# Kernel optimization log

Hardware: AMD Instinct MI355X
Metric: run time of the kernel (lower is better)

## Reference

```python
import jax, jax.numpy as jnp
import numpy as np

_D, _H, _W = 8, 56, 56
WS = 3
PAD = WS // 2
NUM_HEADS = 8
DIM = 128
HEAD_DIM = DIM // NUM_HEADS
LOCAL_LEN = WS ** 3
OFFSETS = [(dz, dy, dx) for dz in range(WS) for dy in range(WS) for dx in range(WS)]


def _mask_and_scale():
    # Replicates get_seqlen_and_mask: which of the 27 neighbors are in-bounds.
    z = np.arange(_D)[:, None, None]
    y = np.arange(_H)[None, :, None]
    x = np.arange(_W)[None, None, :]
    valid = []
    for dz, dy, dx in OFFSETS:
        v = ((z + dz - PAD >= 0) & (z + dz - PAD < _D) &
             (y + dy - PAD >= 0) & (y + dy - PAD < _H) &
             (x + dx - PAD >= 0) & (x + dx - PAD < _W))
        valid.append(np.broadcast_to(v, (_D, _H, _W)).reshape(-1))
    valid = np.stack(valid, -1)  # [N, 27]
    pad_mask = jnp.asarray(~valid)  # True where neighbor is padding
    seq_scale = jnp.asarray(np.log(valid.sum(-1).astype(np.float32))[:, None])  # [N, 1]
    return pad_mask, seq_scale

PAD_MASK, SEQ_SCALE = _mask_and_scale()


def _l2norm(t):
    # F.normalize(dim=-1) with eps=1e-12
    return t / jnp.maximum(jnp.linalg.norm(t, axis=-1, keepdims=True), 1e-12)


def setup_inputs() -> dict:
    key = jax.random.key(0)
    ks = jax.random.split(key, 8)
    B, N, C = 4, _D * _H * _W, DIM
    s = 0.02
    return {
        "x": jax.random.normal(ks[0], (B, N, C), jnp.float32),
        "q_w": jax.random.normal(ks[1], (C, C), jnp.float32) * s,
        "q_b": jnp.zeros((C,), jnp.float32),
        "kv_w": jax.random.normal(ks[2], (2 * C, C), jnp.float32) * s,
        "kv_b": jnp.zeros((2 * C,), jnp.float32),
        "proj_w": jax.random.normal(ks[3], (C, C), jnp.float32) * s,
        "proj_b": jnp.zeros((C,), jnp.float32),
        "temperature": jnp.log(jnp.expm1(jnp.ones((NUM_HEADS, 1, 1), jnp.float32) / 0.24)),
        "query_embedding": jax.random.normal(ks[4], (NUM_HEADS, 1, HEAD_DIM), jnp.float32) * 0.02,
        "rel_pos_bias": jax.random.normal(ks[5], (NUM_HEADS, LOCAL_LEN), jnp.float32) * 0.0004,
        "D": _D, "H": _H, "W": _W,
    }


def reference(x, q_w, q_b, kv_w, kv_b, proj_w, proj_b, temperature,
              query_embedding, rel_pos_bias, D, H, W):
    B, N, C = x.shape
    h, hd = NUM_HEADS, HEAD_DIM

    # q branch: linear -> per-head L2 normalize -> embed/temperature/length scaling
    q = (x @ q_w.T + q_b).reshape(B, N, h, hd).transpose(0, 2, 1, 3)  # [B,h,N,hd]
    q = _l2norm(q)
    q = (q + query_embedding) * jax.nn.softplus(temperature) * SEQ_SCALE

    # kv branch: k L2-normalized per head, v raw
    kv = x @ kv_w.T + kv_b
    k, v = kv[..., :C], kv[..., C:]
    k = _l2norm(k.reshape(B, N, h, hd))
    kmap = k.transpose(0, 2, 3, 1).reshape(B, h, hd, D, H, W)
    vmap = v.reshape(B, N, h, hd).transpose(0, 2, 3, 1).reshape(B, h, hd, D, H, W)
    pad_cfg = [(0, 0)] * 3 + [(PAD, PAD)] * 3
    kpad = jnp.pad(kmap, pad_cfg)
    vpad = jnp.pad(vmap, pad_cfg)

    # QK over 27 shifted views == unfold3d gather without materializing [B,h,hd,27,N]
    attn = []
    for dz, dy, dx in OFFSETS:
        ks = kpad[..., dz:dz + D, dy:dy + H, dx:dx + W].reshape(B, h, hd, N)
        attn.append(jnp.einsum('bhnd,bhdn->bhn', q, ks))
    attn = jnp.stack(attn, -1)  # [B,h,N,27]
    attn = attn + rel_pos_bias[None, :, None, :]
    attn = jnp.where(PAD_MASK[None, None], -jnp.inf, attn)
    attn = jax.nn.softmax(attn, axis=-1)

    # AV accumulation over the same 27 shifts
    out = jnp.zeros((B, h, N, hd), x.dtype)
    for j, (dz, dy, dx) in enumerate(OFFSETS):
        vs = vpad[..., dz:dz + D, dy:dy + H, dx:dx + W].reshape(B, h, hd, N)
        out = out + attn[..., j, None] * vs.transpose(0, 1, 3, 2)
    out = out.transpose(0, 2, 1, 3).reshape(B, N, C)
    return out @ proj_w.T + proj_b
```

## Files before the change

### kernel.cpp

```cpp
#include <hip/hip_runtime.h>

#define DD 8
#define HH 56
#define WW 56
#define HWW (HH*WW)
#define NTOK (DD*HH*WW)
#define BB 4
#define CC 128
#define NH 8
#define HD 16
#define MTOT (BB*NTOK)

__device__ __forceinline__ unsigned short f2bf(float f){
    unsigned int u = __float_as_uint(f);
    u += 0x7FFFu + ((u>>16)&1u);
    return (unsigned short)(u>>16);
}
__device__ __forceinline__ float bf2f(unsigned short s){
    return __uint_as_float(((unsigned int)s)<<16);
}

__global__ __launch_bounds__(256)
void qkv_kernel(const float* __restrict__ x,
                const float* __restrict__ qw, const float* __restrict__ qb,
                const float* __restrict__ kvw, const float* __restrict__ kvb,
                const float* __restrict__ temp, const float* __restrict__ qemb,
                float* __restrict__ qbuf, float* __restrict__ kbuf,
                unsigned short* __restrict__ vbuf)
{
    __shared__ float xs[32*72];
    __shared__ float wsl[32*388];
    const int t = threadIdx.x;
    const int rowbase = blockIdx.x * 64;
    const int r0 = 4*(t>>4);
    const int c0 = 4*(t&15);

    float acc[4][24];
    #pragma unroll
    for (int cc=0; cc<6; ++cc){
        #pragma unroll
        for (int j=0;j<4;++j){
            int col = cc*64 + c0 + j;
            float b = (col<CC) ? qb[col] : kvb[col-CC];
            #pragma unroll
            for (int i=0;i<4;++i) acc[i][cc*4+j]=b;
        }
    }

    for (int ks=0; ks<4; ++ks){
        __syncthreads();
        #pragma unroll
        for (int i=0;i<2;++i){
            int id = 4*t + 1024*i;
            int row = id>>5, k0 = id&31;
            float4 xv = *reinterpret_cast<const float4*>(x + (size_t)(rowbase+row)*CC + ks*32 + k0);
            xs[(k0+0)*72+row]=xv.x; xs[(k0+1)*72+row]=xv.y;
            xs[(k0+2)*72+row]=xv.z; xs[(k0+3)*72+row]=xv.w;
        }
        #pragma unroll
        for (int i=0;i<12;++i){
            int id = 4*t + 1024*i;
            int c = id>>5, k0 = id&31;
            const float* wrow = (c<CC) ? (qw + (size_t)c*CC) : (kvw + (size_t)(c-CC)*CC);
            float4 wv = *reinterpret_cast<const float4*>(wrow + ks*32 + k0);
            wsl[(k0+0)*388+c]=wv.x; wsl[(k0+1)*388+c]=wv.y;
            wsl[(k0+2)*388+c]=wv.z; wsl[(k0+3)*388+c]=wv.w;
        }
        __syncthreads();
        #pragma unroll 4
        for (int k=0;k<32;++k){
            float4 xa = *reinterpret_cast<const float4*>(&xs[k*72 + r0]);
            float xr[4] = {xa.x, xa.y, xa.z, xa.w};
            #pragma unroll
            for (int cc=0;cc<6;++cc){
                float4 wb = *reinterpret_cast<const float4*>(&wsl[k*388 + cc*64 + c0]);
                float wr[4] = {wb.x,wb.y,wb.z,wb.w};
                #pragma unroll
                for (int i=0;i<4;++i){
                    #pragma unroll
                    for (int j=0;j<4;++j)
                        acc[i][cc*4+j] = fmaf(xr[i], wr[j], acc[i][cc*4+j]);
                }
            }
        }
    }

    #pragma unroll
    for (int cc=0; cc<6; ++cc){
        const int sel = cc>>1;
        const int colbase = (cc&1)*64 + c0;
        float vals[4][4];
        #pragma unroll
        for (int i=0;i<4;++i){
            #pragma unroll
            for (int j=0;j<4;++j) vals[i][j]=acc[i][cc*4+j];
        }

        if (sel<2){
            #pragma unroll
            for (int i=0;i<4;++i){
                float s = vals[i][0]*vals[i][0]+vals[i][1]*vals[i][1]
                        + vals[i][2]*vals[i][2]+vals[i][3]*vals[i][3];
                s += __shfl_xor(s,1);
                s += __shfl_xor(s,2);
                float inv = 1.0f/fmaxf(sqrtf(s),1e-12f);
                #pragma unroll
                for (int j=0;j<4;++j) vals[i][j]*=inv;
            }
        }
        if (sel==0){
            const int head = colbase>>4;
            const int d0 = colbase&15;
            float tm = temp[head];
            float sps = (tm>15.f)?tm:log1pf(__expf(tm));
            float qe[4];
            #pragma unroll
            for (int j=0;j<4;++j) qe[j]=qemb[head*HD + d0 + j];
            #pragma unroll
            for (int i=0;i<4;++i){
                int row = rowbase + r0 + i;
                int n = row % NTOK;
                int z = n / HWW; int rem = n - z*HWW;
                int y = rem / WW; int xx = rem - y*WW;
                int cnt = (3-(z==0)-(z==DD-1))*(3-(y==0)-(y==HH-1))*(3-(xx==0)-(xx==WW-1));
                float sc = logf((float)cnt) * sps;
                #pragma unroll
                for (int j=0;j<4;++j) vals[i][j]=(vals[i][j]+qe[j])*sc;
            }
        }
        #pragma unroll
        for (int i=0;i<4;++i){
            int row = rowbase + r0 + i;
            if (sel==0){
                *reinterpret_cast<float4*>(qbuf + (size_t)row*CC + colbase)
                    = make_float4(vals[i][0],vals[i][1],vals[i][2],vals[i][3]);
            } else if (sel==1){
                *reinterpret_cast<float4*>(kbuf + (size_t)row*CC + colbase)
                    = make_float4(vals[i][0],vals[i][1],vals[i][2],vals[i][3]);
            } else {
                *reinterpret_cast<ushort4*>(vbuf + (size_t)row*CC + colbase)
                    = make_ushort4(f2bf(vals[i][0]),f2bf(vals[i][1]),f2bf(vals[i][2]),f2bf(vals[i][3]));
            }
        }
    }
}

__global__ __launch_bounds__(256)
void attn_kernel(float* __restrict__ qa,
                 const float* __restrict__ kbuf,
                 const unsigned short* __restrict__ vbuf,
                 const float* __restrict__ rpb)
{
    const int t = threadIdx.x;
    const int tok = blockIdx.x*32 + (t>>3);
    const int h = t&7;
    const int n = tok % NTOK;
    const int z = n / HWW; const int rem = n - z*HWW;
    const int y = rem / WW; const int xx = rem - y*WW;
    const int tokbase = tok - n;

    float qf[16];
    {
        const float4* qp = reinterpret_cast<const float4*>(qa + (size_t)tok*CC + h*HD);
        float4 a=qp[0],b=qp[1],c=qp[2],d=qp[3];
        qf[0]=a.x;qf[1]=a.y;qf[2]=a.z;qf[3]=a.w;
        qf[4]=b.x;qf[5]=b.y;qf[6]=b.z;qf[7]=b.w;
        qf[8]=c.x;qf[9]=c.y;qf[10]=c.z;qf[11]=c.w;
        qf[12]=d.x;qf[13]=d.y;qf[14]=d.z;qf[15]=d.w;
    }

    float l[27];
    #pragma unroll
    for (int j=0;j<27;++j){
        const int dz=j/9, dy=(j/3)%3, dx=j%3;
        int z2=z+dz-1, y2=y+dy-1, x2=xx+dx-1;
        bool valid = ((unsigned)z2<DD) && ((unsigned)y2<HH) && ((unsigned)x2<WW);
        int row2 = valid ? (tokbase + z2*HWW + y2*WW + x2) : tok;
        const float4* kp = reinterpret_cast<const float4*>(kbuf + (size_t)row2*CC + h*HD);
        float4 ka=kp[0],kb=kp[1],kc=kp[2],kd=kp[3];
        float kk[16]={ka.x,ka.y,ka.z,ka.w, kb.x,kb.y,kb.z,kb.w,
                      kc.x,kc.y,kc.z,kc.w, kd.x,kd.y,kd.z,kd.w};
        float s = 0.f;
        #pragma unroll
        for (int d=0;d<16;++d) s = fmaf(qf[d],kk[d],s);
        l[j] = valid ? (s + rpb[h*27+j]) : -1e30f;
    }

    float m = l[0];
    #pragma unroll
    for (int j=1;j<27;++j) m = fmaxf(m,l[j]);
    float sum=0.f;
    #pragma unroll
    for (int j=0;j<27;++j){ float e=__expf(l[j]-m); l[j]=e; sum+=e; }
    float rs = 1.0f/sum;

    float o[16];
    #pragma unroll
    for (int d=0;d<16;++d) o[d]=0.f;
    #pragma unroll
    for (int j=0;j<27;++j){
        const int dz=j/9, dy=(j/3)%3, dx=j%3;
        int z2=z+dz-1, y2=y+dy-1, x2=xx+dx-1;
        bool valid = ((unsigned)z2<DD) && ((unsigned)y2<HH) && ((unsigned)x2<WW);
        int row2 = valid ? (tokbase + z2*HWW + y2*WW + x2) : tok;
        const uint4* vp = reinterpret_cast<const uint4*>(vbuf + (size_t)row2*CC + h*HD);
        uint4 va=vp[0], vb=vp[1];
        unsigned int vw[8]={va.x,va.y,va.z,va.w,vb.x,vb.y,vb.z,vb.w};
        float w = l[j];
        #pragma unroll
        for (int q2=0;q2<8;++q2){
            o[2*q2]   = fmaf(w, bf2f((unsigned short)(vw[q2]&0xffffu)), o[2*q2]);
            o[2*q2+1] = fmaf(w, bf2f((unsigned short)(vw[q2]>>16)),     o[2*q2+1]);
        }
    }
    #pragma unroll
    for (int d=0;d<16;++d) o[d]*=rs;
    float4* op = reinterpret_cast<float4*>(qa + (size_t)tok*CC + h*HD);
    op[0]=make_float4(o[0],o[1],o[2],o[3]);
    op[1]=make_float4(o[4],o[5],o[6],o[7]);
    op[2]=make_float4(o[8],o[9],o[10],o[11]);
    op[3]=make_float4(o[12],o[13],o[14],o[15]);
}

__global__ __launch_bounds__(256)
void proj_kernel(const float* __restrict__ ao, const float* __restrict__ pw,
                 const float* __restrict__ pb, float* __restrict__ out)
{
    __shared__ float xs[32*72];
    __shared__ float wsl[32*132];
    const int t = threadIdx.x;
    const int rowbase = blockIdx.x*64;
    const int r0 = 4*(t>>4);
    const int c0 = 8*(t&15);
    float acc[4][8];
    #pragma unroll
    for (int j=0;j<8;++j){
        float b=pb[c0+j];
        #pragma unroll
        for (int i=0;i<4;++i) acc[i][j]=b;
    }
    for (int ks=0;ks<4;++ks){
        __syncthreads();
        #pragma unroll
        for (int i=0;i<2;++i){
            int id=4*t+1024*i; int row=id>>5,k0=id&31;
            float4 xv = *reinterpret_cast<const float4*>(ao + (size_t)(rowbase+row)*CC + ks*32 + k0);
            xs[(k0+0)*72+row]=xv.x; xs[(k0+1)*72+row]=xv.y;
            xs[(k0+2)*72+row]=xv.z; xs[(k0+3)*72+row]=xv.w;
        }
        #pragma unroll
        for (int i=0;i<4;++i){
            int id=4*t+1024*i; int c=id>>5,k0=id&31;
            float4 wv = *reinterpret_cast<const float4*>(pw + (size_t)c*CC + ks*32 + k0);
            wsl[(k0+0)*132+c]=wv.x; wsl[(k0+1)*132+c]=wv.y;
            wsl[(k0+2)*132+c]=wv.z; wsl[(k0+3)*132+c]=wv.w;
        }
        __syncthreads();
        #pragma unroll 4
        for (int k=0;k<32;++k){
            float4 xa=*reinterpret_cast<const float4*>(&xs[k*72+r0]);
            float xr[4]={xa.x,xa.y,xa.z,xa.w};
            float4 w0=*reinterpret_cast<const float4*>(&wsl[k*132+c0]);
            float4 w1=*reinterpret_cast<const float4*>(&wsl[k*132+c0+4]);
            float wr[8]={w0.x,w0.y,w0.z,w0.w,w1.x,w1.y,w1.z,w1.w};
            #pragma unroll
            for (int i=0;i<4;++i){
                #pragma unroll
                for (int j=0;j<8;++j)
                    acc[i][j] = fmaf(xr[i], wr[j], acc[i][j]);
            }
        }
    }
    #pragma unroll
    for (int i=0;i<4;++i){
        int row=rowbase+r0+i;
        *reinterpret_cast<float4*>(out+(size_t)row*CC+c0)
            = make_float4(acc[i][0],acc[i][1],acc[i][2],acc[i][3]);
        *reinterpret_cast<float4*>(out+(size_t)row*CC+c0+4)
            = make_float4(acc[i][4],acc[i][5],acc[i][6],acc[i][7]);
    }
}

extern "C" void kernel_launch(void* const* d_in, const int* in_sizes, int n_in,
                              void* d_out, int out_size, void* d_ws, size_t ws_size,
                              hipStream_t stream)
{
    const float* x    = (const float*)d_in[0];
    const float* qw   = (const float*)d_in[1];
    const float* qb   = (const float*)d_in[2];
    const float* kvw  = (const float*)d_in[3];
    const float* kvb  = (const float*)d_in[4];
    const float* pw   = (const float*)d_in[5];
    const float* pb   = (const float*)d_in[6];
    const float* temp = (const float*)d_in[7];
    const float* qemb = (const float*)d_in[8];
    const float* rpb  = (const float*)d_in[9];

    float* qbuf = (float*)d_ws;
    float* kbuf = qbuf + (size_t)MTOT*CC;
    unsigned short* vbuf = (unsigned short*)(kbuf + (size_t)MTOT*CC);

    hipLaunchKernelGGL(qkv_kernel, dim3(MTOT/64), dim3(256), 0, stream,
                       x,qw,qb,kvw,kvb,temp,qemb,qbuf,kbuf,vbuf);
    hipLaunchKernelGGL(attn_kernel, dim3(MTOT/32), dim3(256), 0, stream,
                       qbuf,kbuf,vbuf,rpb);
    hipLaunchKernelGGL(proj_kernel, dim3(MTOT/64), dim3(256), 0, stream,
                       qbuf,pw,pb,(float*)d_out);
}
```

Before: 485.9 us.

## Use split-bf16 MFMA for QKV and output projection GEMMs

Replaces the scalar FP32 FMA GEMMs in the qkv and projection kernels with bf16 MFMA 16x16x32 instructions. Precision is kept close to FP32 by splitting operands into hi/lo bf16 parts, using three MFMAs per tile. A small pre-kernel splits the weights each call, and activations are split in registers without shared memory staging. This trades FP32 ALU work for matrix-core throughput, at the cost of an extra launch, strided scalar stores in the epilogue, and an approximation slightly less exact than FP32.

```diff
diff --git a/kernel.cpp b/kernel.cpp
--- a/kernel.cpp
+++ b/kernel.cpp
@@ -11,6 +11,9 @@
 #define HD 16
 #define MTOT (BB*NTOK)
 
+typedef __attribute__((ext_vector_type(8))) short bf16x8;
+typedef __attribute__((ext_vector_type(4))) float f32x4;
+
 __device__ __forceinline__ unsigned short f2bf(float f){
     unsigned int u = __float_as_uint(f);
     u += 0x7FFFu + ((u>>16)&1u);
@@ -21,125 +24,144 @@
 }
 
 __global__ __launch_bounds__(256)
+void wsplit_kernel(const float* __restrict__ qw, const float* __restrict__ kvw,
+                   const float* __restrict__ pw,
+                   unsigned short* __restrict__ whi, unsigned short* __restrict__ wlo,
+                   unsigned short* __restrict__ pwhi, unsigned short* __restrict__ pwlo)
+{
+    int idx = blockIdx.x*256 + threadIdx.x;
+    if (idx < 49152){
+        float s = (idx < 16384) ? qw[idx] : kvw[idx-16384];
+        unsigned short h = f2bf(s);
+        unsigned short l = f2bf(s - bf2f(h));
+        whi[idx]=h; wlo[idx]=l;
+    } else {
+        int j = idx - 49152;
+        float s = pw[j];
+        unsigned short h = f2bf(s);
+        unsigned short l = f2bf(s - bf2f(h));
+        pwhi[j]=h; pwlo[j]=l;
+    }
+}
+
+__global__ __launch_bounds__(256)
 void qkv_kernel(const float* __restrict__ x,
-                const float* __restrict__ qw, const float* __restrict__ qb,
-                const float* __restrict__ kvw, const float* __restrict__ kvb,
+                const float* __restrict__ qb, const float* __restrict__ kvb,
+                const unsigned short* __restrict__ whi, const unsigned short* __restrict__ wlo,
                 const float* __restrict__ temp, const float* __restrict__ qemb,
                 float* __restrict__ qbuf, float* __restrict__ kbuf,
                 unsigned short* __restrict__ vbuf)
 {
-    __shared__ float xs[32*72];
-    __shared__ float wsl[32*388];
-    const int t = threadIdx.x;
-    const int rowbase = blockIdx.x * 64;
-    const int r0 = 4*(t>>4);
-    const int c0 = 4*(t&15);
-
-    float acc[4][24];
-    #pragma unroll
-    for (int cc=0; cc<6; ++cc){
-        #pragma unroll
-        for (int j=0;j<4;++j){
-            int col = cc*64 + c0 + j;
-            float b = (col<CC) ? qb[col] : kvb[col-CC];
-            #pragma unroll
-            for (int i=0;i<4;++i) acc[i][cc*4+j]=b;
-        }
-    }
-
+    const int t  = threadIdx.x;
+    const int wv = t>>6;
+    const int l  = t&63;
+    const int lr = l&15;
+    const int lg = l>>4;
+    const int m0 = blockIdx.x*64;
+
+    f32x4 acc[4][6];
+    #pragma unroll
+    for (int j=0;j<6;++j){
+        int col = (wv*6+j)*16 + lr;
+        float b = (col<CC) ? qb[col] : kvb[col-CC];
+        #pragma unroll
+        for (int rt=0;rt<4;++rt) acc[rt][j] = (f32x4){b,b,b,b};
+    }
+
+    #pragma unroll
     for (int ks=0; ks<4; ++ks){
-        __syncthreads();
-        #pragma unroll
-        for (int i=0;i<2;++i){
-            int id = 4*t + 1024*i;
-            int row = id>>5, k0 = id&31;
-            float4 xv = *reinterpret_cast<const float4*>(x + (size_t)(rowbase+row)*CC + ks*32 + k0);
-            xs[(k0+0)*72+row]=xv.x; xs[(k0+1)*72+row]=xv.y;
-            xs[(k0+2)*72+row]=xv.z; xs[(k0+3)*72+row]=xv.w;
-        }
-        #pragma unroll
-        for (int i=0;i<12;++i){
-            int id = 4*t + 1024*i;
-            int c = id>>5, k0 = id&31;
-            const float* wrow = (c<CC) ? (qw + (size_t)c*CC) : (kvw + (size_t)(c-CC)*CC);
-            float4 wv = *reinterpret_cast<const float4*>(wrow + ks*32 + k0);
-            wsl[(k0+0)*388+c]=wv.x; wsl[(k0+1)*388+c]=wv.y;
-            wsl[(k0+2)*388+c]=wv.z; wsl[(k0+3)*388+c]=wv.w;
-        }
-        __syncthreads();
-        #pragma unroll 4
-        for (int k=0;k<32;++k){
-            float4 xa = *reinterpret_cast<const float4*>(&xs[k*72 + r0]);
-            float xr[4] = {xa.x, xa.y, xa.z, xa.w};
-            #pragma unroll
-            for (int cc=0;cc<6;++cc){
-                float4 wb = *reinterpret_cast<const float4*>(&wsl[k*388 + cc*64 + c0]);
-                float wr[4] = {wb.x,wb.y,wb.z,wb.w};
+        bf16x8 ahi[4], alo[4];
+        #pragma unroll
+        for (int rt=0;rt<4;++rt){
+            const float* xp = x + (size_t)(m0 + rt*16 + lr)*CC + ks*32 + lg*8;
+            float4 xa = *reinterpret_cast<const float4*>(xp);
+            float4 xb = *reinterpret_cast<const float4*>(xp+4);
+            float xf[8] = {xa.x,xa.y,xa.z,xa.w, xb.x,xb.y,xb.z,xb.w};
+            #pragma unroll
+            for (int jj=0;jj<8;++jj){
+                unsigned short h = f2bf(xf[jj]);
+                unsigned short lo2 = f2bf(xf[jj] - bf2f(h));
+                ahi[rt][jj] = (short)h;
+                alo[rt][jj] = (short)lo2;
+            }
+        }
+        #pragma unroll
+        for (int j=0;j<6;++j){
+            const int c = (wv*6+j)*16 + lr;
+            const size_t off = (size_t)c*CC + ks*32 + lg*8;
+            bf16x8 bhi = *reinterpret_cast<const bf16x8*>(whi + off);
+            bf16x8 blo = *reinterpret_cast<const bf16x8*>(wlo + off);
+            #pragma unroll
+            for (int rt=0;rt<4;++rt){
+                acc[rt][j] = __builtin_amdgcn_mfma_f32_16x16x32_bf16(ahi[rt], bhi, acc[rt][j], 0,0,0);
+                acc[rt][j] = __builtin_amdgcn_mfma_f32_16x16x32_bf16(alo[rt], bhi, acc[rt][j], 0,0,0);
+                acc[rt][j] = __builtin_amdgcn_mfma_f32_16x16x32_bf16(ahi[rt], blo, acc[rt][j], 0,0,0);
+            }
+        }
+    }
+
+    float slog[4][4];
+    #pragma unroll
+    for (int rt=0;rt<4;++rt){
+        #pragma unroll
+        for (int r=0;r<4;++r){
+            int row = m0 + rt*16 + lg*4 + r;
+            int n = row % NTOK;
+            int z = n / HWW; int rem = n - z*HWW;
+            int y = rem / WW; int xx = rem - y*WW;
+            const float L2 = 0.69314718f, L3 = 1.09861229f;
+            float sl = ((z==0||z==DD-1)?L2:L3) + ((y==0||y==HH-1)?L2:L3) + ((xx==0||xx==WW-1)?L2:L3);
+            slog[rt][r] = sl;
+        }
+    }
+
+    #pragma unroll
+    for (int j=0;j<6;++j){
+        const int ct  = wv*6+j;
+        const int sel = ct>>3;
+        const int head = ct & 7;
+        float vals[4][4];
+        #pragma unroll
+        for (int rt=0;rt<4;++rt){
+            #pragma unroll
+            for (int r=0;r<4;++r) vals[rt][r] = acc[rt][j][r];
+        }
+        if (sel < 2){
+            #pragma unroll
+            for (int rt=0;rt<4;++rt){
                 #pragma unroll
-                for (int i=0;i<4;++i){
-                    #pragma unroll
-                    for (int j=0;j<4;++j)
-                        acc[i][cc*4+j] = fmaf(xr[i], wr[j], acc[i][cc*4+j]);
+                for (int r=0;r<4;++r){
+                    float s = vals[rt][r]*vals[rt][r];
+                    s += __shfl_xor(s,1); s += __shfl_xor(s,2);
+                    s += __shfl_xor(s,4); s += __shfl_xor(s,8);
+                    float inv = 1.0f/fmaxf(sqrtf(s),1e-12f);
+                    vals[rt][r] *= inv;
                 }
             }
         }
-    }
-
-    #pragma unroll
-    for (int cc=0; cc<6; ++cc){
-        const int sel = cc>>1;
-        const int colbase = (cc&1)*64 + c0;
-        float vals[4][4];
-        #pragma unroll
-        for (int i=0;i<4;++i){
-            #pragma unroll
-            for (int j=0;j<4;++j) vals[i][j]=acc[i][cc*4+j];
-        }
-
-        if (sel<2){
-            #pragma unroll
-            for (int i=0;i<4;++i){
-                float s = vals[i][0]*vals[i][0]+vals[i][1]*vals[i][1]
-                        + vals[i][2]*vals[i][2]+vals[i][3]*vals[i][3];
-                s += __shfl_xor(s,1);
-                s += __shfl_xor(s,2);
-                float inv = 1.0f/fmaxf(sqrtf(s),1e-12f);
-                #pragma unroll
-                for (int j=0;j<4;++j) vals[i][j]*=inv;
-            }
-        }
-        if (sel==0){
-            const int head = colbase>>4;
-            const int d0 = colbase&15;
+        if (sel == 0){
             float tm = temp[head];
             float sps = (tm>15.f)?tm:log1pf(__expf(tm));
-            float qe[4];
-            #pragma unroll
-            for (int j=0;j<4;++j) qe[j]=qemb[head*HD + d0 + j];
-            #pragma unroll
-            for (int i=0;i<4;++i){
-                int row = rowbase + r0 + i;
-                int n = row % NTOK;
-                int z = n / HWW; int rem = n - z*HWW;
-                int y = rem / WW; int xx = rem - y*WW;
-                int cnt = (3-(z==0)-(z==DD-1))*(3-(y==0)-(y==HH-1))*(3-(xx==0)-(xx==WW-1));
-                float sc = logf((float)cnt) * sps;
+            float qe = qemb[head*HD + lr];
+            #pragma unroll
+            for (int rt=0;rt<4;++rt){
                 #pragma unroll
-                for (int j=0;j<4;++j) vals[i][j]=(vals[i][j]+qe[j])*sc;
-            }
-        }
-        #pragma unroll
-        for (int i=0;i<4;++i){
-            int row = rowbase + r0 + i;
-            if (sel==0){
-                *reinterpret_cast<float4*>(qbuf + (size_t)row*CC + colbase)
-                    = make_float4(vals[i][0],vals[i][1],vals[i][2],vals[i][3]);
-            } else if (sel==1){
-                *reinterpret_cast<float4*>(kbuf + (size_t)row*CC + colbase)
-                    = make_float4(vals[i][0],vals[i][1],vals[i][2],vals[i][3]);
-            } else {
-                *reinterpret_cast<ushort4*>(vbuf + (size_t)row*CC + colbase)
-                    = make_ushort4(f2bf(vals[i][0]),f2bf(vals[i][1]),f2bf(vals[i][2]),f2bf(vals[i][3]));
+                for (int r=0;r<4;++r)
+                    vals[rt][r] = (vals[rt][r]+qe)*(slog[rt][r]*sps);
+            }
+        }
+        #pragma unroll
+        for (int rt=0;rt<4;++rt){
+            #pragma unroll
+            for (int r=0;r<4;++r){
+                int row = m0 + rt*16 + lg*4 + r;
+                if (sel==0){
+                    qbuf[(size_t)row*CC + ct*16 + lr] = vals[rt][r];
+                } else if (sel==1){
+                    kbuf[(size_t)row*CC + (ct-8)*16 + lr] = vals[rt][r];
+                } else {
+                    vbuf[(size_t)row*CC + (ct-16)*16 + lr] = f2bf(vals[rt][r]);
+                }
             }
         }
     }
@@ -223,61 +245,68 @@
 }
 
 __global__ __launch_bounds__(256)
-void proj_kernel(const float* __restrict__ ao, const float* __restrict__ pw,
+void proj_kernel(const float* __restrict__ ao,
+                 const unsigned short* __restrict__ pwhi, const unsigned short* __restrict__ pwlo,
                  const float* __restrict__ pb, float* __restrict__ out)
 {
-    __shared__ float xs[32*72];
-    __shared__ float wsl[32*132];
-    const int t = threadIdx.x;
-    const int rowbase = blockIdx.x*64;
-    const int r0 = 4*(t>>4);
-    const int c0 = 8*(t&15);
-    float acc[4][8];
-    #pragma unroll
-    for (int j=0;j<8;++j){
-        float b=pb[c0+j];
-        #pragma unroll
-        for (int i=0;i<4;++i) acc[i][j]=b;
-    }
-    for (int ks=0;ks<4;++ks){
-        __syncthreads();
-        #pragma unroll
-        for (int i=0;i<2;++i){
-            int id=4*t+1024*i; int row=id>>5,k0=id&31;
-            float4 xv = *reinterpret_cast<const float4*>(ao + (size_t)(rowbase+row)*CC + ks*32 + k0);
-            xs[(k0+0)*72+row]=xv.x; xs[(k0+1)*72+row]=xv.y;
-            xs[(k0+2)*72+row]=xv.z; xs[(k0+3)*72+row]=xv.w;
-        }
-        #pragma unroll
-        for (int i=0;i<4;++i){
-            int id=4*t+1024*i; int c=id>>5,k0=id&31;
-            float4 wv = *reinterpret_cast<const float4*>(pw + (size_t)c*CC + ks*32 + k0);
-            wsl[(k0+0)*132+c]=wv.x; wsl[(k0+1)*132+c]=wv.y;
-            wsl[(k0+2)*132+c]=wv.z; wsl[(k0+3)*132+c]=wv.w;
-        }
-        __syncthreads();
-        #pragma unroll 4
-        for (int k=0;k<32;++k){
-            float4 xa=*reinterpret_cast<const float4*>(&xs[k*72+r0]);
-            float xr[4]={xa.x,xa.y,xa.z,xa.w};
-            float4 w0=*reinterpret_cast<const float4*>(&wsl[k*132+c0]);
-            float4 w1=*reinterpret_cast<const float4*>(&wsl[k*132+c0+4]);
-            float wr[8]={w0.x,w0.y,w0.z,w0.w,w1.x,w1.y,w1.z,w1.w};
-            #pragma unroll
-            for (int i=0;i<4;++i){
-                #pragma unroll
-                for (int j=0;j<8;++j)
-                    acc[i][j] = fmaf(xr[i], wr[j], acc[i][j]);
-            }
-        }
-    }
-    #pragma unroll
-    for (int i=0;i<4;++i){
-        int row=rowbase+r0+i;
-        *reinterpret_cast<float4*>(out+(size_t)row*CC+c0)
-            = make_float4(acc[i][0],acc[i][1],acc[i][2],acc[i][3]);
-        *reinterpret_cast<float4*>(out+(size_t)row*CC+c0+4)
-            = make_float4(acc[i][4],acc[i][5],acc[i][6],acc[i][7]);
+    const int t  = threadIdx.x;
+    const int wv = t>>6;
+    const int l  = t&63;
+    const int lr = l&15;
+    const int lg = l>>4;
+    const int m0 = blockIdx.x*64;
+
+    f32x4 acc[4][2];
+    #pragma unroll
+    for (int j=0;j<2;++j){
+        float b = pb[(wv*2+j)*16 + lr];
+        #pragma unroll
+        for (int rt=0;rt<4;++rt) acc[rt][j] = (f32x4){b,b,b,b};
+    }
+
+    #pragma unroll
+    for (int ks=0; ks<4; ++ks){
+        bf16x8 ahi[4], alo[4];
+        #pragma unroll
+        for (int rt=0;rt<4;++rt){
+            const float* xp = ao + (size_t)(m0 + rt*16 + lr)*CC + ks*32 + lg*8;
+            float4 xa = *reinterpret_cast<const float4*>(xp);
+            float4 xb = *reinterpret_cast<const float4*>(xp+4);
+            float xf[8] = {xa.x,xa.y,xa.z,xa.w, xb.x,xb.y,xb.z,xb.w};
+            #pragma unroll
+            for (int jj=0;jj<8;++jj){
+                unsigned short h = f2bf(xf[jj]);
+                unsigned short lo2 = f2bf(xf[jj] - bf2f(h));
+                ahi[rt][jj] = (short)h;
+                alo[rt][jj] = (short)lo2;
+            }
+        }
+        #pragma unroll
+        for (int j=0;j<2;++j){
+            const int c = (wv*2+j)*16 + lr;
+            const size_t off = (size_t)c*CC + ks*32 + lg*8;
+            bf16x8 bhi = *reinterpret_cast<const bf16x8*>(pwhi + off);
+            bf16x8 blo = *reinterpret_cast<const bf16x8*>(pwlo + off);
+            #pragma unroll
+            for (int rt=0;rt<4;++rt){
+                acc[rt][j] = __builtin_amdgcn_mfma_f32_16x16x32_bf16(ahi[rt], bhi, acc[rt][j], 0,0,0);
+                acc[rt][j] = __builtin_amdgcn_mfma_f32_16x16x32_bf16(alo[rt], bhi, acc[rt][j], 0,0,0);
+                acc[rt][j] = __builtin_amdgcn_mfma_f32_16x16x32_bf16(ahi[rt], blo, acc[rt][j], 0,0,0);
+            }
+        }
+    }
+
+    #pragma unroll
+    for (int j=0;j<2;++j){
+        const int col = (wv*2+j)*16 + lr;
+        #pragma unroll
+        for (int rt=0;rt<4;++rt){
+            #pragma unroll
+            for (int r=0;r<4;++r){
+                int row = m0 + rt*16 + lg*4 + r;
+                out[(size_t)row*CC + col] = acc[rt][j][r];
+            }
+        }
     }
 }
 
@@ -299,11 +328,17 @@
     float* qbuf = (float*)d_ws;
     float* kbuf = qbuf + (size_t)MTOT*CC;
     unsigned short* vbuf = (unsigned short*)(kbuf + (size_t)MTOT*CC);
-
+    unsigned short* whi  = vbuf + (size_t)MTOT*CC;
+    unsigned short* wlo  = whi + 384*CC;
+    unsigned short* pwhi = wlo + 384*CC;
+    unsigned short* pwlo = pwhi + CC*CC;
+
+    hipLaunchKernelGGL(wsplit_kernel, dim3(256), dim3(256), 0, stream,
+                       qw,kvw,pw,whi,wlo,pwhi,pwlo);
     hipLaunchKernelGGL(qkv_kernel, dim3(MTOT/64), dim3(256), 0, stream,
-                       x,qw,qb,kvw,kvb,temp,qemb,qbuf,kbuf,vbuf);
+                       x,qb,kvb,whi,wlo,temp,qemb,qbuf,kbuf,vbuf);
     hipLaunchKernelGGL(attn_kernel, dim3(MTOT/32), dim3(256), 0, stream,
                        qbuf,kbuf,vbuf,rpb);
     hipLaunchKernelGGL(proj_kernel, dim3(MTOT/64), dim3(256), 0, stream,
-                       qbuf,pw,pb,(float*)d_out);
-}
+                       qbuf,pwhi,pwlo,pb,(float*)d_out);
+}
```

Result: slower. 648.7 us (+33.5%).
